# Performance work log

Measured on AMD Instinct MI355X. Metric: run time of the kernel, lower is better.

The kernel has to match this reference:

```python
import jax, jax.numpy as jnp
import numpy as np

K_PRED = 6
SCORE_TEMPERATURE = 0.5
NMS_THRESH = np.array([2.5, 1.0, 1.5], dtype=np.float32)  # [veh, ped, cyc] meters
SUPPRESSED_SCORE = 0.001


def setup_inputs() -> dict:
    key = jax.random.key(0)
    k0, k1, k2, k3 = jax.random.split(key, 4)
    D, S, A, P, T = 1, 64, 128, 6, 80  # n_decoder, n_scene, n_agent, n_pred, n_step_future
    pred_valid = jnp.ones((S, A), dtype=bool)
    pred_conf = jax.random.normal(k0, (D, S, A, P), dtype=jnp.float32)
    # scale positions to realistic meters so distances straddle the NMS thresholds
    pred_pos = jax.random.normal(k1, (D, S, A, P, T, 2), dtype=jnp.float32) * 10.0
    pred_yaw_bbox = jax.random.normal(k2, (D, S, A, P, T, 1), dtype=jnp.float32)
    type_idx = jax.random.randint(k3, (S, A), 0, 3)
    ref_type = jax.nn.one_hot(type_idx, 3, dtype=jnp.float32)
    return {
        'pred_valid': pred_valid,
        'pred_conf': pred_conf,
        'pred_pos': pred_pos,
        'pred_yaw_bbox': pred_yaw_bbox,
        'ref_type': ref_type,
    }


def _nms_one_agent(scores, within, valid):
    # scores: [K], within: [K, K] bool, valid: scalar bool
    order = jnp.argsort(-scores)  # descending, computed once on original scores

    def step(cur, k):
        # suppress k if any other prediction within distance has a (currently) higher score
        mask = within[k] & (cur > cur[k])
        new_val = jnp.where(jnp.any(mask), jnp.asarray(SUPPRESSED_SCORE, cur.dtype), cur[k])
        return cur.at[k].set(new_val), None

    out, _ = jax.lax.scan(step, scores, order)
    return jnp.where(valid, out, scores)


_nms = jax.vmap(jax.vmap(_nms_one_agent))  # over scene, agent


def reference(pred_valid, pred_conf, pred_pos, pred_yaw_bbox, ref_type):
    D, S, A, P, T, _ = pred_pos.shape
    K = D * P
    # [n_scene, n_agent, k_pred, n_step, 2]
    trajs = jnp.moveaxis(pred_pos, 0, 2).reshape(S, A, K, T, 2)
    scores = jax.nn.softmax(pred_conf, axis=-1)
    scores = jnp.moveaxis(scores, 0, 2).reshape(S, A, K)
    scores = scores / jnp.sum(scores, axis=-1, keepdims=True)

    # mpa_nms: per-agent-type distance threshold
    thresh = jnp.einsum('sat,t->sa', ref_type, jnp.asarray(NMS_THRESH))[:, :, None, None]
    # use_ade=True: mean pairwise distance over time -> [S, A, K, K]
    diff = trajs[:, :, :, None] - trajs[:, :, None, :]          # [S,A,K,K,T,2]
    within_dist = jnp.mean(jnp.linalg.norm(diff, axis=-1), axis=-1) < thresh
    scores = _nms(scores, within_dist, pred_valid)
    scores = scores / jnp.sum(scores, axis=-1, keepdims=True)

    # score temperature
    scores = jax.nn.softmax(jnp.log(scores) / SCORE_TEMPERATURE, axis=-1)

    waymo_trajs = jnp.moveaxis(trajs, 3, 1)                      # [S, T, A, K, 2]
    waymo_scores = scores                                        # [S, A, K]
    waymo_valid = jnp.broadcast_to(pred_valid[:, None, :], (S, T, A))
    yaw_bbox = jnp.moveaxis(pred_yaw_bbox, 0, 2).reshape(S, A, K, T, 1)
    waymo_yaw_bbox = jnp.moveaxis(yaw_bbox, 3, 1)                # [S, T, A, K, 1]
    return waymo_valid, waymo_trajs, waymo_scores, waymo_yaw_bbox
```

## Files before the change

kernel.cpp:

```cpp
#include <hip/hip_runtime.h>
#include <hip/hip_bf16.h>

#define NS 64
#define NA 128
#define NK 6
#define NT 80

#define OFF_TRAJ   655360
#define OFF_SCORE  (655360 + 7864320)
#define OFF_YAW    (655360 + 7864320 + 49152)

typedef float nfloat4 __attribute__((ext_vector_type(4)));

#define APS 82

__global__ __launch_bounds__(256) void waymo_pos_kernel(
    const int*    __restrict__ validIn,
    const float*  __restrict__ confIn,
    const float2* __restrict__ posIn,
    const float*  __restrict__ typeIn,
    float*        __restrict__ out)
{
    const int s   = blockIdx.y;
    const int a0  = blockIdx.x * 4;
    const int tid = threadIdx.x;

    __shared__ float2 sP[24 * APS];

    const size_t sa0 = (size_t)s * NA + a0;
    const float2* pbase = posIn + sa0 * (NK * NT);

    for (int i = tid; i < 960; i += 256) {
        int r = i / 40, q = i - r * 40;
        nfloat4 v = *(const nfloat4*)(pbase + (size_t)r * NT + 2 * q);
        *(nfloat4*)&sP[r * APS + 2 * q] = v;
    }
    __syncthreads();

    if (tid < 128) {
        const int la   = tid >> 5;
        const int lane = tid & 31;
        const int p    = lane >> 1;
        const int half = lane & 1;

        const size_t sa = (size_t)s * NA + a0 + la;
        const float th = 2.5f * typeIn[sa * 3 + 0]
                       + 1.0f * typeIn[sa * 3 + 1]
                       + 1.5f * typeIn[sa * 3 + 2];

        int pi, pj;
        if      (p < 5)  { pi = 0; pj = p + 1; }
        else if (p < 9)  { pi = 1; pj = p - 3; }
        else if (p < 12) { pi = 2; pj = p - 6; }
        else if (p < 14) { pi = 3; pj = p - 8; }
        else             { pi = 4; pj = 5;     }

        const int rI = la * NK + pi, rJ = la * NK + pj;
        float dsum = 0.f;
        for (int t = half * 40; t < half * 40 + 40; ++t) {
            float2 u = sP[rI * APS + t];
            float2 v = sP[rJ * APS + t];
            float dx = u.x - v.x, dy = u.y - v.y;
            dsum += sqrtf(dx * dx + dy * dy);
        }
        dsum += __shfl_xor(dsum, 1);
        const bool within = (dsum / 80.0f) < th;
        const bool predb  = (half == 0) && (p < 15) && within;
        unsigned long long bal = __ballot(predb);
        unsigned mask32 = (unsigned)(bal >> (tid & 32));

        if (lane == 0) {
            float c[NK];
            float mx = -3e38f;
            for (int q = 0; q < NK; ++q) { c[q] = confIn[sa * NK + q]; mx = fmaxf(mx, c[q]); }
            float ssum = 0.f;
            for (int q = 0; q < NK; ++q) { c[q] = expf(c[q] - mx); ssum += c[q]; }
            for (int q = 0; q < NK; ++q) c[q] /= ssum;
            ssum = 0.f;
            for (int q = 0; q < NK; ++q) ssum += c[q];
            for (int q = 0; q < NK; ++q) c[q] /= ssum;

            int ord[NK]; bool used[NK];
            for (int q = 0; q < NK; ++q) used[q] = false;
            for (int st = 0; st < NK; ++st) {
                int best = 0; float bv = -3e38f;
                for (int q = 0; q < NK; ++q)
                    if (!used[q] && c[q] > bv) { bv = c[q]; best = q; }
                used[best] = true; ord[st] = best;
            }

            float cur[NK];
            for (int q = 0; q < NK; ++q) cur[q] = c[q];

            if (validIn[sa] != 0) {
                for (int st = 0; st < NK; ++st) {
                    int k = ord[st];
                    float ck = cur[k];
                    bool any = false;
                    for (int j = 0; j < NK; ++j) {
                        if (j == k) continue;
                        int lo = j < k ? j : k;
                        int hi = j < k ? k : j;
                        int pidx = lo * 5 - (lo * (lo - 1)) / 2 + (hi - lo - 1);
                        if (((mask32 >> (2 * pidx)) & 1u) && (cur[j] > ck)) any = true;
                    }
                    if (any) cur[k] = 0.001f;
                }
            }

            float tsum = 0.f;
            for (int q = 0; q < NK; ++q) tsum += cur[q];
            float w[NK]; float wsum = 0.f;
            for (int q = 0; q < NK; ++q) {
                float qq = cur[q] / tsum;
                w[q] = qq * qq; wsum += w[q];
            }
            float* outSc = out + OFF_SCORE;
            for (int q = 0; q < NK; ++q) outSc[sa * NK + q] = w[q] / wsum;
        }
    }

    nfloat4* trajOut = (nfloat4*)(out + OFF_TRAJ);
    for (int o = tid; o < 960; o += 256) {
        int t = o / 12, j = o - (o / 12) * 12;
        float2 u = sP[(2 * j + 0) * APS + t];
        float2 w = sP[(2 * j + 1) * APS + t];
        nfloat4 v{u.x, u.y, w.x, w.y};
        size_t f4 = (size_t)(s * NT + t) * 384 + a0 * 3 + j;
        trajOut[f4] = v;
    }
}

#define BYS 84

__global__ __launch_bounds__(256) void waymo_yaw_kernel(
    const float* __restrict__ yawIn,
    float*       __restrict__ out)
{
    const int s   = blockIdx.y;
    const int a0  = blockIdx.x * 8;
    const int tid = threadIdx.x;

    __shared__ float sY[48 * BYS];

    const size_t sa0 = (size_t)s * NA + a0;
    const float* ybase = yawIn + sa0 * (NK * NT);

    for (int i = tid; i < 960; i += 256) {
        int r = i / 20, m = i - r * 20;
        nfloat4 v = *(const nfloat4*)(ybase + (size_t)r * NT + 4 * m);
        *(nfloat4*)&sY[r * BYS + 4 * m] = v;
    }
    __syncthreads();

    nfloat4* yawOut = (nfloat4*)(out + OFF_YAW);
    for (int o = tid; o < 960; o += 256) {
        int t = o / 12, j = o - (o / 12) * 12;
        nfloat4 v{sY[(4 * j + 0) * BYS + t],
                  sY[(4 * j + 1) * BYS + t],
                  sY[(4 * j + 2) * BYS + t],
                  sY[(4 * j + 3) * BYS + t]};
        size_t f4 = (size_t)(s * NT + t) * 192 + ((a0 * 6) >> 2) + j;
        yawOut[f4] = v;
    }
}

__global__ __launch_bounds__(256) void waymo_valid_kernel(
    const int* __restrict__ validIn,
    float*     __restrict__ out)
{
    const int s   = blockIdx.x;
    const int tid = threadIdx.x;

    __shared__ nfloat4 vrow[NA / 4];

    if (tid < 32) {
        const int b = (int)((size_t)s * NA) + 4 * tid;
        nfloat4 v;
        v.x = (validIn[b + 0] != 0) ? 1.0f : 0.0f;
        v.y = (validIn[b + 1] != 0) ? 1.0f : 0.0f;
        v.z = (validIn[b + 2] != 0) ? 1.0f : 0.0f;
        v.w = (validIn[b + 3] != 0) ? 1.0f : 0.0f;
        vrow[tid] = v;
    }
    __syncthreads();

    nfloat4* vOut = (nfloat4*)out;
    for (int o = tid; o < NT * 32; o += 256) {
        int t = o >> 5, q = o & 31;
        vOut[(size_t)(s * NT + t) * 32 + q] = vrow[q];
    }
}

extern "C" void kernel_launch(void* const* d_in, const int* in_sizes, int n_in,
                              void* d_out, int out_size, void* d_ws, size_t ws_size,
                              hipStream_t stream) {
    const int*    validIn = (const int*)d_in[0];
    const float*  confIn  = (const float*)d_in[1];
    const float2* posIn   = (const float2*)d_in[2];
    const float*  yawIn   = (const float*)d_in[3];
    const float*  typeIn  = (const float*)d_in[4];
    float* out = (float*)d_out;

    dim3 gridA(NA / 4, NS);
    waymo_pos_kernel<<<gridA, 256, 0, stream>>>(validIn, confIn, posIn, typeIn, out);
    dim3 gridB(NA / 8, NS);
    waymo_yaw_kernel<<<gridB, 256, 0, stream>>>(yawIn, out);
    waymo_valid_kernel<<<NS, 256, 0, stream>>>(validIn, out);
}
```

Baseline: 38.80 us.

## Split trajectory transpose from NMS scoring and tile transposes over time chunks

Trajectory transposition moves into its own kernel that tiles over 64 agents by 8 time steps, so each block writes long contiguous output rows instead of short 4-agent segments. The valid broadcast is folded into the yaw transpose kernel, which now uses the same agent-half by time-chunk tiling, so one launch is removed. NMS scoring becomes a separate kernel with 8 agents per block and all 256 threads computing distances. The cost is that the position input is read twice, once for the transpose and once for scoring.

Measured after the change: 55.26 us. +42.4%, slower.

```diff
diff --git a/kernel.cpp b/kernel.cpp
--- a/kernel.cpp
+++ b/kernel.cpp
@@ -12,183 +12,192 @@
 
 typedef float nfloat4 __attribute__((ext_vector_type(4)));
 
-#define APS 82
-
-__global__ __launch_bounds__(256) void waymo_pos_kernel(
+#define PW 388
+
+__global__ __launch_bounds__(256) void k_traj(
+    const float2* __restrict__ posIn,
+    float*        __restrict__ out)
+{
+    const int s   = blockIdx.y;
+    const int bx  = blockIdx.x;
+    const int ah  = bx & 1;
+    const int tc  = bx >> 1;
+    const int a0  = ah * 64;
+    const int t0  = tc * 8;
+    const int tid = threadIdx.x;
+
+    __shared__ float2 sPT[8][PW];
+
+    const float2* pbase = posIn + ((size_t)s * NA + a0) * (NK * NT);
+
+    for (int i = tid; i < 1536; i += 256) {
+        int r = i >> 2, c = i & 3;
+        nfloat4 v = *(const nfloat4*)(pbase + (size_t)r * NT + t0 + 2 * c);
+        sPT[2 * c + 0][r] = float2{v.x, v.y};
+        sPT[2 * c + 1][r] = float2{v.z, v.w};
+    }
+    __syncthreads();
+
+    nfloat4* trajOut = (nfloat4*)(out + OFF_TRAJ);
+    for (int o = tid; o < 1536; o += 256) {
+        int t = o / 192, j = o - (o / 192) * 192;
+        nfloat4 v = *(const nfloat4*)&sPT[t][2 * j];
+        trajOut[(size_t)(s * NT + t0 + t) * 384 + ah * 192 + j] = v;
+    }
+}
+
+#define YW 392
+
+__global__ __launch_bounds__(256) void k_yaw(
+    const int*   __restrict__ validIn,
+    const float* __restrict__ yawIn,
+    float*       __restrict__ out)
+{
+    const int s   = blockIdx.y;
+    const int bx  = blockIdx.x;
+    const int ah  = bx & 1;
+    const int tc  = bx >> 1;
+    const int a0  = ah * 64;
+    const int t0  = tc * 8;
+    const int tid = threadIdx.x;
+
+    __shared__ float sYT[8][YW];
+
+    const float* ybase = yawIn + ((size_t)s * NA + a0) * (NK * NT);
+
+    if (ah == 0) {
+        int t = tid >> 5, q = tid & 31;
+        const int b = s * NA + 4 * q;
+        nfloat4 v;
+        v.x = (validIn[b + 0] != 0) ? 1.0f : 0.0f;
+        v.y = (validIn[b + 1] != 0) ? 1.0f : 0.0f;
+        v.z = (validIn[b + 2] != 0) ? 1.0f : 0.0f;
+        v.w = (validIn[b + 3] != 0) ? 1.0f : 0.0f;
+        ((nfloat4*)out)[(size_t)(s * NT + t0 + t) * 32 + q] = v;
+    }
+
+    for (int i = tid; i < 768; i += 256) {
+        int r = i >> 1, c = i & 1;
+        nfloat4 v = *(const nfloat4*)(ybase + (size_t)r * NT + t0 + 4 * c);
+        sYT[4 * c + 0][r] = v.x;
+        sYT[4 * c + 1][r] = v.y;
+        sYT[4 * c + 2][r] = v.z;
+        sYT[4 * c + 3][r] = v.w;
+    }
+    __syncthreads();
+
+    nfloat4* yawOut = (nfloat4*)(out + OFF_YAW);
+    for (int o = tid; o < 768; o += 256) {
+        int t = o / 96, j = o - (o / 96) * 96;
+        nfloat4 v = *(const nfloat4*)&sYT[t][4 * j];
+        yawOut[(size_t)(s * NT + t0 + t) * 192 + ah * 96 + j] = v;
+    }
+}
+
+#define SPS 82
+
+__global__ __launch_bounds__(256) void k_score(
     const int*    __restrict__ validIn,
     const float*  __restrict__ confIn,
     const float2* __restrict__ posIn,
     const float*  __restrict__ typeIn,
     float*        __restrict__ out)
 {
-    const int s   = blockIdx.y;
-    const int a0  = blockIdx.x * 4;
+    const int g   = blockIdx.x;
     const int tid = threadIdx.x;
-
-    __shared__ float2 sP[24 * APS];
-
-    const size_t sa0 = (size_t)s * NA + a0;
-    const float2* pbase = posIn + sa0 * (NK * NT);
-
-    for (int i = tid; i < 960; i += 256) {
+    const int s   = g >> 4;
+    const int a0  = (g & 15) * 8;
+
+    __shared__ float2 sPos[48 * SPS];
+
+    const float2* pbase = posIn + ((size_t)s * NA + a0) * (NK * NT);
+
+    for (int i = tid; i < 1920; i += 256) {
         int r = i / 40, q = i - r * 40;
         nfloat4 v = *(const nfloat4*)(pbase + (size_t)r * NT + 2 * q);
-        *(nfloat4*)&sP[r * APS + 2 * q] = v;
+        *(nfloat4*)&sPos[r * SPS + 2 * q] = v;
     }
     __syncthreads();
 
-    if (tid < 128) {
-        const int la   = tid >> 5;
-        const int lane = tid & 31;
-        const int p    = lane >> 1;
-        const int half = lane & 1;
-
-        const size_t sa = (size_t)s * NA + a0 + la;
-        const float th = 2.5f * typeIn[sa * 3 + 0]
-                       + 1.0f * typeIn[sa * 3 + 1]
-                       + 1.5f * typeIn[sa * 3 + 2];
-
-        int pi, pj;
-        if      (p < 5)  { pi = 0; pj = p + 1; }
-        else if (p < 9)  { pi = 1; pj = p - 3; }
-        else if (p < 12) { pi = 2; pj = p - 6; }
-        else if (p < 14) { pi = 3; pj = p - 8; }
-        else             { pi = 4; pj = 5;     }
-
-        const int rI = la * NK + pi, rJ = la * NK + pj;
-        float dsum = 0.f;
-        for (int t = half * 40; t < half * 40 + 40; ++t) {
-            float2 u = sP[rI * APS + t];
-            float2 v = sP[rJ * APS + t];
-            float dx = u.x - v.x, dy = u.y - v.y;
-            dsum += sqrtf(dx * dx + dy * dy);
+    const int la   = tid >> 5;
+    const int lane = tid & 31;
+    const int p    = lane >> 1;
+    const int half = lane & 1;
+
+    const size_t sa = (size_t)s * NA + a0 + la;
+    const float th = 2.5f * typeIn[sa * 3 + 0]
+                   + 1.0f * typeIn[sa * 3 + 1]
+                   + 1.5f * typeIn[sa * 3 + 2];
+
+    int pi, pj;
+    if      (p < 5)  { pi = 0; pj = p + 1; }
+    else if (p < 9)  { pi = 1; pj = p - 3; }
+    else if (p < 12) { pi = 2; pj = p - 6; }
+    else if (p < 14) { pi = 3; pj = p - 8; }
+    else             { pi = 4; pj = 5;     }
+
+    const int rI = la * NK + pi, rJ = la * NK + pj;
+    float dsum = 0.f;
+    for (int t = half * 40; t < half * 40 + 40; ++t) {
+        float2 u = sPos[rI * SPS + t];
+        float2 v = sPos[rJ * SPS + t];
+        float dx = u.x - v.x, dy = u.y - v.y;
+        dsum += sqrtf(dx * dx + dy * dy);
+    }
+    dsum += __shfl_xor(dsum, 1);
+    const bool within = (dsum / 80.0f) < th;
+    const bool predb  = (half == 0) && (p < 15) && within;
+    unsigned long long bal = __ballot(predb);
+    unsigned mask32 = (unsigned)(bal >> (tid & 32));
+
+    if (lane == 0) {
+        float c[NK];
+        float mx = -3e38f;
+        for (int q = 0; q < NK; ++q) { c[q] = confIn[sa * NK + q]; mx = fmaxf(mx, c[q]); }
+        float ssum = 0.f;
+        for (int q = 0; q < NK; ++q) { c[q] = expf(c[q] - mx); ssum += c[q]; }
+        for (int q = 0; q < NK; ++q) c[q] /= ssum;
+        ssum = 0.f;
+        for (int q = 0; q < NK; ++q) ssum += c[q];
+        for (int q = 0; q < NK; ++q) c[q] /= ssum;
+
+        int ord[NK]; bool used[NK];
+        for (int q = 0; q < NK; ++q) used[q] = false;
+        for (int st = 0; st < NK; ++st) {
+            int best = 0; float bv = -3e38f;
+            for (int q = 0; q < NK; ++q)
+                if (!used[q] && c[q] > bv) { bv = c[q]; best = q; }
+            used[best] = true; ord[st] = best;
         }
-        dsum += __shfl_xor(dsum, 1);
-        const bool within = (dsum / 80.0f) < th;
-        const bool predb  = (half == 0) && (p < 15) && within;
-        unsigned long long bal = __ballot(predb);
-        unsigned mask32 = (unsigned)(bal >> (tid & 32));
-
-        if (lane == 0) {
-            float c[NK];
-            float mx = -3e38f;
-            for (int q = 0; q < NK; ++q) { c[q] = confIn[sa * NK + q]; mx = fmaxf(mx, c[q]); }
-            float ssum = 0.f;
-            for (int q = 0; q < NK; ++q) { c[q] = expf(c[q] - mx); ssum += c[q]; }
-            for (int q = 0; q < NK; ++q) c[q] /= ssum;
-            ssum = 0.f;
-            for (int q = 0; q < NK; ++q) ssum += c[q];
-            for (int q = 0; q < NK; ++q) c[q] /= ssum;
-
-            int ord[NK]; bool used[NK];
-            for (int q = 0; q < NK; ++q) used[q] = false;
+
+        float cur[NK];
+        for (int q = 0; q < NK; ++q) cur[q] = c[q];
+
+        if (validIn[sa] != 0) {
             for (int st = 0; st < NK; ++st) {
-                int best = 0; float bv = -3e38f;
-                for (int q = 0; q < NK; ++q)
-                    if (!used[q] && c[q] > bv) { bv = c[q]; best = q; }
-                used[best] = true; ord[st] = best;
+                int k = ord[st];
+                float ck = cur[k];
+                bool any = false;
+                for (int j = 0; j < NK; ++j) {
+                    if (j == k) continue;
+                    int lo = j < k ? j : k;
+                    int hi = j < k ? k : j;
+                    int pidx = lo * 5 - (lo * (lo - 1)) / 2 + (hi - lo - 1);
+                    if (((mask32 >> (2 * pidx)) & 1u) && (cur[j] > ck)) any = true;
+                }
+                if (any) cur[k] = 0.001f;
             }
-
-            float cur[NK];
-            for (int q = 0; q < NK; ++q) cur[q] = c[q];
-
-            if (validIn[sa] != 0) {
-                for (int st = 0; st < NK; ++st) {
-                    int k = ord[st];
-                    float ck = cur[k];
-                    bool any = false;
-                    for (int j = 0; j < NK; ++j) {
-                        if (j == k) continue;
-                        int lo = j < k ? j : k;
-                        int hi = j < k ? k : j;
-                        int pidx = lo * 5 - (lo * (lo - 1)) / 2 + (hi - lo - 1);
-                        if (((mask32 >> (2 * pidx)) & 1u) && (cur[j] > ck)) any = true;
-                    }
-                    if (any) cur[k] = 0.001f;
-                }
-            }
-
-            float tsum = 0.f;
-            for (int q = 0; q < NK; ++q) tsum += cur[q];
-            float w[NK]; float wsum = 0.f;
-            for (int q = 0; q < NK; ++q) {
-                float qq = cur[q] / tsum;
-                w[q] = qq * qq; wsum += w[q];
-            }
-            float* outSc = out + OFF_SCORE;
-            for (int q = 0; q < NK; ++q) outSc[sa * NK + q] = w[q] / wsum;
         }
-    }
-
-    nfloat4* trajOut = (nfloat4*)(out + OFF_TRAJ);
-    for (int o = tid; o < 960; o += 256) {
-        int t = o / 12, j = o - (o / 12) * 12;
-        float2 u = sP[(2 * j + 0) * APS + t];
-        float2 w = sP[(2 * j + 1) * APS + t];
-        nfloat4 v{u.x, u.y, w.x, w.y};
-        size_t f4 = (size_t)(s * NT + t) * 384 + a0 * 3 + j;
-        trajOut[f4] = v;
-    }
-}
-
-#define BYS 84
-
-__global__ __launch_bounds__(256) void waymo_yaw_kernel(
-    const float* __restrict__ yawIn,
-    float*       __restrict__ out)
-{
-    const int s   = blockIdx.y;
-    const int a0  = blockIdx.x * 8;
-    const int tid = threadIdx.x;
-
-    __shared__ float sY[48 * BYS];
-
-    const size_t sa0 = (size_t)s * NA + a0;
-    const float* ybase = yawIn + sa0 * (NK * NT);
-
-    for (int i = tid; i < 960; i += 256) {
-        int r = i / 20, m = i - r * 20;
-        nfloat4 v = *(const nfloat4*)(ybase + (size_t)r * NT + 4 * m);
-        *(nfloat4*)&sY[r * BYS + 4 * m] = v;
-    }
-    __syncthreads();
-
-    nfloat4* yawOut = (nfloat4*)(out + OFF_YAW);
-    for (int o = tid; o < 960; o += 256) {
-        int t = o / 12, j = o - (o / 12) * 12;
-        nfloat4 v{sY[(4 * j + 0) * BYS + t],
-                  sY[(4 * j + 1) * BYS + t],
-                  sY[(4 * j + 2) * BYS + t],
-                  sY[(4 * j + 3) * BYS + t]};
-        size_t f4 = (size_t)(s * NT + t) * 192 + ((a0 * 6) >> 2) + j;
-        yawOut[f4] = v;
-    }
-}
-
-__global__ __launch_bounds__(256) void waymo_valid_kernel(
-    const int* __restrict__ validIn,
-    float*     __restrict__ out)
-{
-    const int s   = blockIdx.x;
-    const int tid = threadIdx.x;
-
-    __shared__ nfloat4 vrow[NA / 4];
-
-    if (tid < 32) {
-        const int b = (int)((size_t)s * NA) + 4 * tid;
-        nfloat4 v;
-        v.x = (validIn[b + 0] != 0) ? 1.0f : 0.0f;
-        v.y = (validIn[b + 1] != 0) ? 1.0f : 0.0f;
-        v.z = (validIn[b + 2] != 0) ? 1.0f : 0.0f;
-        v.w = (validIn[b + 3] != 0) ? 1.0f : 0.0f;
-        vrow[tid] = v;
-    }
-    __syncthreads();
-
-    nfloat4* vOut = (nfloat4*)out;
-    for (int o = tid; o < NT * 32; o += 256) {
-        int t = o >> 5, q = o & 31;
-        vOut[(size_t)(s * NT + t) * 32 + q] = vrow[q];
+
+        float tsum = 0.f;
+        for (int q = 0; q < NK; ++q) tsum += cur[q];
+        float w[NK]; float wsum = 0.f;
+        for (int q = 0; q < NK; ++q) {
+            float qq = cur[q] / tsum;
+            w[q] = qq * qq; wsum += w[q];
+        }
+        float* outSc = out + OFF_SCORE;
+        for (int q = 0; q < NK; ++q) outSc[sa * NK + q] = w[q] / wsum;
     }
 }
 
@@ -202,9 +211,9 @@
     const float*  typeIn  = (const float*)d_in[4];
     float* out = (float*)d_out;
 
-    dim3 gridA(NA / 4, NS);
-    waymo_pos_kernel<<<gridA, 256, 0, stream>>>(validIn, confIn, posIn, typeIn, out);
-    dim3 gridB(NA / 8, NS);
-    waymo_yaw_kernel<<<gridB, 256, 0, stream>>>(yawIn, out);
-    waymo_valid_kernel<<<NS, 256, 0, stream>>>(validIn, out);
-}
+    dim3 gridT(20, NS);
+    k_traj<<<gridT, 256, 0, stream>>>(posIn, out);
+    dim3 gridY(20, NS);
+    k_yaw<<<gridY, 256, 0, stream>>>(validIn, yawIn, out);
+    k_score<<<1024, 256, 0, stream>>>(validIn, confIn, posIn, typeIn, out);
+}
```
